# Performance work log

Measured on AMD Instinct MI355X. Metric: run time of the kernel, lower is better.

## Reference

```python
import jax, jax.numpy as jnp
import numpy as np


def _patch_size(w):
    # mirrors PatchLoss size selection (static shape -> Python branch is fine)
    if w == 512:
        return 64
    elif 256 <= w < 512:
        return 32
    raise ValueError('error size')


def setup_inputs() -> dict:
    key = jax.random.key(0)
    k1, k2 = jax.random.split(key)
    shape = (1, 3, 32, 512, 512)  # (b=1, c, t, h, w)
    x = jax.random.normal(k1, shape, dtype=jnp.float32)
    x_r = jax.random.normal(k2, shape, dtype=jnp.float32)
    return {"x": x, "x_r": x_r}


def reference(x, x_r):
    _, c, t, h, w = x.shape
    size = _patch_size(w)
    tc, hc, wc = 1, size // 2, size // 2
    # L = |(x+1)/2 - (x_r+1)/2| ; original detaches before pooling
    L = jnp.abs((x + 1.0) / 2.0 - (x_r + 1.0) / 2.0)
    D = jax.lax.stop_gradient(L)[0]  # (c, t, h, w), batch squeezed
    # patch means over (c, hc, wc) for each frame (tc=1) and spatial block
    nh, nw = h // hc, w // wc
    P = D.reshape(c, t, nh, hc, nw, wc).mean(axis=(0, 3, 5))  # (t, nh, nw)
    # max over spatial patches; original init max_patch=0.0, so clamp at 0
    max_patches = jnp.maximum(P.max(axis=(1, 2)), 0.0)  # (t,)
    return jnp.log(max_patches.mean())
```

## Files before the change

kernel.cpp:

```cpp
#include <hip/hip_runtime.h>
#include <math.h>


#define CC 3
#define TT 32
#define HH 512
#define WW 512
#define NPATCH 8192

__global__ __launch_bounds__(256) void patch_sum_kernel(
    const float* __restrict__ x, const float* __restrict__ xr,
    float* __restrict__ patch) {
  const int pidx = blockIdx.x;
  const int t  = pidx >> 8;
  const int ph = (pidx >> 4) & 15;
  const int pw = pidx & 15;
  const int tid = threadIdx.x;
  const int row = tid >> 3;
  const int col = (tid & 7) << 2;

  float acc = 0.f;
#pragma unroll
  for (int ch = 0; ch < CC; ++ch) {
    size_t off = ((size_t)(ch * TT + t) * HH + (size_t)(ph * 32 + row)) * WW
               + (size_t)(pw * 32 + col);
    float4 a = *(const float4*)(x + off);
    float4 b = *(const float4*)(xr + off);
    acc += fabsf(a.x - b.x) + fabsf(a.y - b.y)
         + fabsf(a.z - b.z) + fabsf(a.w - b.w);
  }

#pragma unroll
  for (int o = 32; o > 0; o >>= 1) acc += __shfl_down(acc, o, 64);
  __shared__ float s[4];
  if ((tid & 63) == 0) s[tid >> 6] = acc;
  __syncthreads();
  if (tid == 0) {
    float tot = s[0] + s[1] + s[2] + s[3];
    patch[pidx] = tot * (0.5f / 3072.0f);
  }
}

__global__ __launch_bounds__(256) void finalize_kernel(
    const float* __restrict__ patch, float* __restrict__ out) {
  const int tid = threadIdx.x;
  __shared__ float s[4];
  float total = 0.f;
  for (int t = 0; t < TT; ++t) {
    float v = patch[t * 256 + tid];
#pragma unroll
    for (int o = 32; o > 0; o >>= 1) v = fmaxf(v, __shfl_down(v, o, 64));
    if ((tid & 63) == 0) s[tid >> 6] = v;
    __syncthreads();
    if (tid == 0) {
      float m = fmaxf(fmaxf(s[0], s[1]), fmaxf(s[2], s[3]));
      total += fmaxf(m, 0.f);
    }
    __syncthreads();
  }
  if (tid == 0) out[0] = logf(total / (float)TT);
}

extern "C" void kernel_launch(void* const* d_in, const int* in_sizes, int n_in,
                              void* d_out, int out_size, void* d_ws, size_t ws_size,
                              hipStream_t stream) {
  const float* x  = (const float*)d_in[0];
  const float* xr = (const float*)d_in[1];
  float* patch = (float*)d_ws;
  float* out   = (float*)d_out;

  patch_sum_kernel<<<NPATCH, 256, 0, stream>>>(x, xr, patch);
  finalize_kernel<<<1, 256, 0, stream>>>(patch, out);
}
```

Baseline: 232.6 us.

## Stream contiguous row bands per block and reduce per-patch partials in finalize

Each block now reads 32 contiguous full-width rows of one channel/frame with coalesced float4 loads, 16 per thread, instead of a 32x32 patch across three channels. Per-patch partial sums are produced through 8-lane shuffles and shared atomics. The finalize kernel sums the channels, takes the max, and averages in parallel with 1024 threads. The goal is to cut scattered short-row accesses and raise bytes in flight per thread, at the cost of a larger partial buffer and shared-memory atomics.

```diff
diff --git a/kernel.cpp b/kernel.cpp
--- a/kernel.cpp
+++ b/kernel.cpp
@@ -2,63 +2,60 @@
 #include <math.h>
 
 
-#define CC 3
-#define TT 32
-#define HH 512
-#define WW 512
-#define NPATCH 8192
+#define NPART 8192
 
 __global__ __launch_bounds__(256) void patch_sum_kernel(
     const float* __restrict__ x, const float* __restrict__ xr,
-    float* __restrict__ patch) {
-  const int pidx = blockIdx.x;
-  const int t  = pidx >> 8;
-  const int ph = (pidx >> 4) & 15;
-  const int pw = pidx & 15;
+    float* __restrict__ part) {
+  const int b  = blockIdx.x;
   const int tid = threadIdx.x;
-  const int row = tid >> 3;
-  const int col = (tid & 7) << 2;
+  const size_t base = ((size_t)(b >> 4) * 512 + (size_t)(b & 15) * 32) * 512;
+  const float4* __restrict__ a4 = (const float4*)(x  + base);
+  const float4* __restrict__ b4 = (const float4*)(xr + base);
 
   float acc = 0.f;
-#pragma unroll
-  for (int ch = 0; ch < CC; ++ch) {
-    size_t off = ((size_t)(ch * TT + t) * HH + (size_t)(ph * 32 + row)) * WW
-               + (size_t)(pw * 32 + col);
-    float4 a = *(const float4*)(x + off);
-    float4 b = *(const float4*)(xr + off);
-    acc += fabsf(a.x - b.x) + fabsf(a.y - b.y)
-         + fabsf(a.z - b.z) + fabsf(a.w - b.w);
+#pragma unroll 8
+  for (int i = 0; i < 16; ++i) {
+    float4 a = a4[i * 256 + tid];
+    float4 c = b4[i * 256 + tid];
+    acc += fabsf(a.x - c.x) + fabsf(a.y - c.y)
+         + fabsf(a.z - c.z) + fabsf(a.w - c.w);
   }
 
-#pragma unroll
-  for (int o = 32; o > 0; o >>= 1) acc += __shfl_down(acc, o, 64);
-  __shared__ float s[4];
-  if ((tid & 63) == 0) s[tid >> 6] = acc;
+  __shared__ float s[16];
+  if (tid < 16) s[tid] = 0.f;
   __syncthreads();
-  if (tid == 0) {
-    float tot = s[0] + s[1] + s[2] + s[3];
-    patch[pidx] = tot * (0.5f / 3072.0f);
-  }
+  acc += __shfl_down(acc, 4, 8);
+  acc += __shfl_down(acc, 2, 8);
+  acc += __shfl_down(acc, 1, 8);
+  if ((tid & 7) == 0) atomicAdd(&s[(tid & 127) >> 3], acc);
+  __syncthreads();
+  if (tid < 16) part[(size_t)b * 16 + tid] = s[tid];
 }
 
-__global__ __launch_bounds__(256) void finalize_kernel(
-    const float* __restrict__ patch, float* __restrict__ out) {
+__global__ __launch_bounds__(1024) void finalize_kernel(
+    const float* __restrict__ part, float* __restrict__ out) {
   const int tid = threadIdx.x;
-  __shared__ float s[4];
-  float total = 0.f;
-  for (int t = 0; t < TT; ++t) {
-    float v = patch[t * 256 + tid];
+  const int t = tid >> 5;
+  const int j = tid & 31;
+  float m = -1e30f;
 #pragma unroll
-    for (int o = 32; o > 0; o >>= 1) v = fmaxf(v, __shfl_down(v, o, 64));
-    if ((tid & 63) == 0) s[tid >> 6] = v;
-    __syncthreads();
-    if (tid == 0) {
-      float m = fmaxf(fmaxf(s[0], s[1]), fmaxf(s[2], s[3]));
-      total += fmaxf(m, 0.f);
-    }
-    __syncthreads();
+  for (int k = 0; k < 8; ++k) {
+    int p = t * 256 + j + 32 * k;
+    float v = part[p] + part[NPART + p] + part[2 * NPART + p];
+    m = fmaxf(m, v);
   }
-  if (tid == 0) out[0] = logf(total / (float)TT);
+#pragma unroll
+  for (int o = 16; o > 0; o >>= 1) m = fmaxf(m, __shfl_down(m, o, 32));
+  __shared__ float s[32];
+  if (j == 0) s[t] = fmaxf(m * (0.5f / 3072.0f), 0.f);
+  __syncthreads();
+  if (tid < 32) {
+    float v = s[tid];
+#pragma unroll
+    for (int o = 16; o > 0; o >>= 1) v += __shfl_down(v, o, 32);
+    if (tid == 0) out[0] = logf(v * (1.0f / 32.0f));
+  }
 }
 
 extern "C" void kernel_launch(void* const* d_in, const int* in_sizes, int n_in,
@@ -66,9 +63,9 @@
                               hipStream_t stream) {
   const float* x  = (const float*)d_in[0];
   const float* xr = (const float*)d_in[1];
-  float* patch = (float*)d_ws;
-  float* out   = (float*)d_out;
+  float* part = (float*)d_ws;
+  float* out  = (float*)d_out;
 
-  patch_sum_kernel<<<NPATCH, 256, 0, stream>>>(x, xr, patch);
-  finalize_kernel<<<1, 256, 0, stream>>>(patch, out);
+  patch_sum_kernel<<<1536, 256, 0, stream>>>(x, xr, part);
+  finalize_kernel<<<1, 1024, 0, stream>>>(part, out);
 }
```

Result: faster. 215.4 us (-7.4%).
